# Kernel optimization log

Measured on AMD Instinct MI355X. Metric: run time of the kernel, lower is better.

## Reference

```python
import jax, jax.numpy as jnp
import numpy as np

B, F, S, H = 1024, 64, 512, 128


def setup_inputs() -> dict:
    key = jax.random.key(0)
    ks = jax.random.split(key, 9)
    x = jax.random.normal(ks[0], (B, F, S), dtype=jnp.float32)
    available_len = jax.random.randint(ks[1], (B,), 1, S // 2).astype(jnp.int32)
    extra = jax.random.randint(ks[2], (B,), 0, S // 2)
    predict_len = jnp.minimum(available_len + extra, S).astype(jnp.int32)
    s = 1.0 / float(np.sqrt(H))  # PyTorch default uniform init scale
    u = lambda k, shape: jax.random.uniform(k, shape, jnp.float32, -s, s)
    W_ih = u(ks[3], (4 * H, F))
    W_hh = u(ks[4], (4 * H, H))
    b_ih = u(ks[5], (4 * H,))
    b_hh = u(ks[6], (4 * H,))
    W_den = u(ks[7], (F, H))
    b_den = u(ks[8], (F,))
    init_ch = jnp.zeros((1, 2 * H), dtype=jnp.float32)  # nn.Parameter(zeros(1, 2*n_hidden))
    return {"x": x, "available_len": available_len, "predict_len": predict_len,
            "W_ih": W_ih, "W_hh": W_hh, "b_ih": b_ih, "b_hh": b_hh,
            "W_den": W_den, "b_den": b_den, "init_ch": init_ch}


def reference(x, available_len, predict_len, W_ih, W_hh, b_ih, b_hh, W_den, b_den, init_ch):
    """Masked autoregressive LSTMCell recurrence.

    Row r is active at step t iff t < predict_len[r]; once inactive it never
    re-activates (the torch code's per-step gather of c_1/h_1 by predict_len is
    exactly this monotone-shrinking active set, expressed here as a masked
    full-batch state update). For t >= available_len[r] (and still active) the
    input is the model's own previous prediction (auto-regression feedback).
    Returns the permuted buffer (seq_len, batch, n_fea), matching the torch code.
    """
    Bb, Ff, Ss = x.shape
    Hh = W_hh.shape[1]
    xs = jnp.transpose(x, (2, 0, 1))  # (S, B, F)
    c0 = jnp.broadcast_to(init_ch[:, :Hh], (Bb, Hh))
    h0 = jnp.broadcast_to(init_ch[:, Hh:], (Bb, Hh))

    def step(carry, inp):
        h, c, prev_out = carry
        t, x_t = inp  # t: scalar step index, x_t: (B, F)
        sel = t < predict_len                       # active rows
        use_pred = (t >= available_len) & sel
        inp_t = jnp.where(use_pred[:, None], prev_out, x_t)
        gates = inp_t @ W_ih.T + b_ih + h @ W_hh.T + b_hh  # (B, 4H)
        i, f, g, o = jnp.split(gates, 4, axis=-1)
        c_new = jax.nn.sigmoid(f) * c + jax.nn.sigmoid(i) * jnp.tanh(g)
        h_new = jax.nn.sigmoid(o) * jnp.tanh(c_new)
        h = jnp.where(sel[:, None], h_new, h)
        c = jnp.where(sel[:, None], c_new, c)
        pred = h_new @ W_den.T + b_den              # (B, F)
        out_t = jnp.where(sel[:, None], pred, inp_t)  # x[t, sel] <- prediction
        return (h, c, out_t), out_t

    _, ys = jax.lax.scan(step, (h0, c0, jnp.zeros_like(xs[0])),
                         (jnp.arange(Ss), xs))
    return ys  # (S, B, F)
```

## Files before the change

### kernel.cpp

```cpp
#include <hip/hip_runtime.h>

#define BB 1024
#define FF 64
#define SS 512
#define HH 128
#define ZP 200
#define ZROWS 16
#define OUTS (BB*FF)

typedef __attribute__((ext_vector_type(8))) short bf16x8;
typedef __attribute__((ext_vector_type(4))) float f32x4;

__device__ __forceinline__ unsigned short f2bf(float f) {
    unsigned int u = __float_as_uint(f);
    u += 0x7fff + ((u >> 16) & 1);
    return (unsigned short)(u >> 16);
}

__device__ __forceinline__ void bar_lds() {
    __builtin_amdgcn_sched_barrier(0);
    asm volatile("s_waitcnt lgkmcnt(0)\n\ts_barrier" ::: "memory");
    __builtin_amdgcn_sched_barrier(0);
}

__global__ void fold_kernel(const float* __restrict__ W_ih,
                            const float* __restrict__ W_den,
                            const float* __restrict__ b_den,
                            float* __restrict__ ws)
{
    const int n = blockIdx.x;
    const int k = threadIdx.x;
    float s = 0.f;
    #pragma unroll 8
    for (int f = 0; f < FF; ++f) s = fmaf(W_ih[n*FF + f], W_den[f*HH + k], s);
    ws[n*HH + k] = s;
    if (k == 0) {
        float bsum = 0.f;
        #pragma unroll 8
        for (int f = 0; f < FF; ++f) bsum = fmaf(W_ih[n*FF + f], b_den[f], bsum);
        ws[4*HH*HH + n] = bsum;
    }
}

__global__ void sort_kernel(const int* __restrict__ avail, int* __restrict__ perm)
{
    const int i = threadIdx.x;
    const int key = avail[i];
    int rank = 0;
    for (int j = 0; j < BB; ++j) {
        const int kj = avail[j];
        rank += (kj < key) || (kj == key && j < i);
    }
    perm[rank] = i;
}

__global__ __launch_bounds__(512)
void lstm_mfma_kernel(const float* __restrict__ x,
                      const int* __restrict__ available_len,
                      const int* __restrict__ predict_len,
                      const float* __restrict__ W_ih,
                      const float* __restrict__ W_hh,
                      const float* __restrict__ b_ih,
                      const float* __restrict__ b_hh,
                      const float* __restrict__ W_den,
                      const float* __restrict__ b_den,
                      const float* __restrict__ init_ch,
                      const float* __restrict__ ws,
                      const int* __restrict__ perm,
                      float* __restrict__ out)
{
    const int b0  = blockIdx.x * 4;
    const int tid = threadIdx.x;
    const int w   = tid >> 6;
    const int l   = tid & 63;
    const int l16 = l & 15;
    const int lq  = l >> 4;
    const bool w4 = (w < 4);

    __shared__ __align__(16) unsigned short zbuf[2][ZROWS * ZP];

    for (int i = tid; i < 2 * ZROWS * ZP / 2; i += 512)
        ((unsigned int*)zbuf)[i] = 0u;

    const int rr0 = perm[b0], rr1 = perm[b0+1], rr2 = perm[b0+2], rr3 = perm[b0+3];
    const int p0 = predict_len[rr0], p1 = predict_len[rr1],
              p2 = predict_len[rr2], p3 = predict_len[rr3];
    const int a0i = available_len[rr0], a1i = available_len[rr1],
              a2i = available_len[rr2], a3i = available_len[rr3];
    const int maxP  = max(max(p0, p1), max(p2, p3));
    const int tsw   = max(max(a0i, a1i), max(a2i, a3i));
    const int tmin  = min(min(a0i, a1i), min(a2i, a3i));
    const int ph1s  = (tmin > 1) ? (tmin - 1) : 0;
    const int rl    = perm[b0 + lq];
    const int P_my  = predict_len[rl];
    const int AV_my = available_len[rl];

    bf16x8 wg[4][6];
    float bias[4];
    #pragma unroll
    for (int g = 0; g < 4; ++g) {
        const int n = 128*g + 16*w + l16;
        const float* rih = W_ih + n * FF;
        const float* rhh = W_hh + n * HH;
        #pragma unroll
        for (int kt = 0; kt < 6; ++kt) {
            const int k = 32*kt + 8*lq;
            const float* src = (k < 64) ? (rih + k) : (rhh + (k - 64));
            bf16x8 r;
            #pragma unroll
            for (int i = 0; i < 8; i++) r[i] = (short)f2bf(src[i]);
            wg[g][kt] = r;
        }
        bias[g] = b_ih[n] + b_hh[n];
    }

    bf16x8 wd0, wd1, wd2, wd3;
    float bden = 0.f;
    size_t xbase = 0;
    int AV_x = 0;
    if (w4) {
        const int f = 16*w + l16;
        const float* rd = W_den + f * HH;
        bf16x8 r;
        #pragma unroll
        for (int i = 0; i < 8; i++) r[i] = (short)f2bf(rd[0*32 + 8*lq + i]);
        wd0 = r;
        #pragma unroll
        for (int i = 0; i < 8; i++) r[i] = (short)f2bf(rd[1*32 + 8*lq + i]);
        wd1 = r;
        #pragma unroll
        for (int i = 0; i < 8; i++) r[i] = (short)f2bf(rd[2*32 + 8*lq + i]);
        wd2 = r;
        #pragma unroll
        for (int i = 0; i < 8; i++) r[i] = (short)f2bf(rd[3*32 + 8*lq + i]);
        wd3 = r;
        bden = b_den[f];
        const int rx = perm[b0 + w];
        xbase = ((size_t)rx * FF + l) * SS;
        AV_x  = available_len[rx];
    }

    const int unit  = 16*w + l16;
    const int abase = l16*ZP + 8*lq;
    float c = init_ch[unit];
    const float h0v = init_ch[HH + unit];
    float* outb = out + (size_t)rl * FF + 16*w + l16;

    bar_lds();

    zbuf[0][(4*lq)*ZP + 64 + unit] = f2bf(h0v);
    if (w4) zbuf[0][(4*w)*ZP + l] = f2bf(x[xbase]);

    float4 qc = {0.f,0.f,0.f,0.f};
    if (AV_x > 1) qc = *(const float4*)(x + xbase);

    int cur = 0;

#define DO_T(S, XNEXT)                                                         \
  do {                                                                         \
    const int s_ = (S);                                                        \
    bar_lds();                                             \
    const unsigned short* zc_ = zbuf[cur];                                     \
    bf16x8 a0 = *(const bf16x8*)(zc_ + abase +   0);                           \
    bf16x8 a1 = *(const bf16x8*)(zc_ + abase +  32);                           \
    bf16x8 a2 = *(const bf16x8*)(zc_ + abase +  64);                           \
    bf16x8 a3 = *(const bf16x8*)(zc_ + abase +  96);                           \
    bf16x8 a4 = *(const bf16x8*)(zc_ + abase + 128);                           \
    bf16x8 a5 = *(const bf16x8*)(zc_ + abase + 160);                           \
    if (w4 && s_ >= 1) {                   \
      f32x4 ca = {0.f,0.f,0.f,0.f}, cb = {0.f,0.f,0.f,0.f};                    \
      ca = __builtin_amdgcn_mfma_f32_16x16x32_bf16(a2, wd0, ca, 0,0,0);        \
      cb = __builtin_amdgcn_mfma_f32_16x16x32_bf16(a4, wd2, cb, 0,0,0);        \
      ca = __builtin_amdgcn_mfma_f32_16x16x32_bf16(a3, wd1, ca, 0,0,0);        \
      cb = __builtin_amdgcn_mfma_f32_16x16x32_bf16(a5, wd3, cb, 0,0,0);        \
      if ((s_ - 1) < P_my) outb[(size_t)(s_-1) * OUTS] = ca[0] + cb[0] + bden; \
    }                                                                          \
    f32x4 ac0 = {0.f,0.f,0.f,0.f}, ac1 = {0.f,0.f,0.f,0.f},                    \
          ac2 = {0.f,0.f,0.f,0.f}, ac3 = {0.f,0.f,0.f,0.f};                    \
    ac0 = __builtin_amdgcn_mfma_f32_16x16x32_bf16(a0, wg[0][0], ac0, 0,0,0);   \
    ac1 = __builtin_amdgcn_mfma_f32_16x16x32_bf16(a0, wg[1][0], ac1, 0,0,0);   \
    ac2 = __builtin_amdgcn_mfma_f32_16x16x32_bf16(a0, wg[2][0], ac2, 0,0,0);   \
    ac3 = __builtin_amdgcn_mfma_f32_16x16x32_bf16(a0, wg[3][0], ac3, 0,0,0);   \
    ac0 = __builtin_amdgcn_mfma_f32_16x16x32_bf16(a1, wg[0][1], ac0, 0,0,0);   \
    ac1 = __builtin_amdgcn_mfma_f32_16x16x32_bf16(a1, wg[1][1], ac1, 0,0,0);   \
    ac2 = __builtin_amdgcn_mfma_f32_16x16x32_bf16(a1, wg[2][1], ac2, 0,0,0);   \
    ac3 = __builtin_amdgcn_mfma_f32_16x16x32_bf16(a1, wg[3][1], ac3, 0,0,0);   \
    ac0 = __builtin_amdgcn_mfma_f32_16x16x32_bf16(a2, wg[0][2], ac0, 0,0,0);   \
    ac1 = __builtin_amdgcn_mfma_f32_16x16x32_bf16(a2, wg[1][2], ac1, 0,0,0);   \
    ac2 = __builtin_amdgcn_mfma_f32_16x16x32_bf16(a2, wg[2][2], ac2, 0,0,0);   \
    ac3 = __builtin_amdgcn_mfma_f32_16x16x32_bf16(a2, wg[3][2], ac3, 0,0,0);   \
    ac0 = __builtin_amdgcn_mfma_f32_16x16x32_bf16(a3, wg[0][3], ac0, 0,0,0);   \
    ac1 = __builtin_amdgcn_mfma_f32_16x16x32_bf16(a3, wg[1][3], ac1, 0,0,0);   \
    ac2 = __builtin_amdgcn_mfma_f32_16x16x32_bf16(a3, wg[2][3], ac2, 0,0,0);   \
    ac3 = __builtin_amdgcn_mfma_f32_16x16x32_bf16(a3, wg[3][3], ac3, 0,0,0);   \
    ac0 = __builtin_amdgcn_mfma_f32_16x16x32_bf16(a4, wg[0][4], ac0, 0,0,0);   \
    ac1 = __builtin_amdgcn_mfma_f32_16x16x32_bf16(a4, wg[1][4], ac1, 0,0,0);   \
    ac2 = __builtin_amdgcn_mfma_f32_16x16x32_bf16(a4, wg[2][4], ac2, 0,0,0);   \
    ac3 = __builtin_amdgcn_mfma_f32_16x16x32_bf16(a4, wg[3][4], ac3, 0,0,0);   \
    ac0 = __builtin_amdgcn_mfma_f32_16x16x32_bf16(a5, wg[0][5], ac0, 0,0,0);   \
    ac1 = __builtin_amdgcn_mfma_f32_16x16x32_bf16(a5, wg[1][5], ac1, 0,0,0);   \
    ac2 = __builtin_amdgcn_mfma_f32_16x16x32_bf16(a5, wg[2][5], ac2, 0,0,0);   \
    ac3 = __builtin_amdgcn_mfma_f32_16x16x32_bf16(a5, wg[3][5], ac3, 0,0,0);   \
    const float g0 = ac0[0] + bias[0];                                         \
    const float g1 = ac1[0] + bias[1];                                         \
    const float g2 = ac2[0] + bias[2];                                         \
    const float g3 = ac3[0] + bias[3];                                         \
    const float si = 1.f / (1.f + __expf(-g0));                                \
    const float sf = 1.f / (1.f + __expf(-g1));                                \
    const float tg = 1.f - 2.f / (__expf(2.f * g2) + 1.f);                     \
    const float so = 1.f / (1.f + __expf(-g3));                                \
    const float cn = sf * c + si * tg;                                         \
    const float tc = 1.f - 2.f / (__expf(2.f * cn) + 1.f);                     \
    const float hn = so * tc;                                                  \
    const int nxt_ = cur ^ 1;                                                  \
    if (s_ < P_my) { c = cn; zbuf[nxt_][(4*lq)*ZP + 64 + unit] = f2bf(hn); }   \
    if (w4 && (s_ + 1 < AV_x)) zbuf[nxt_][(4*w)*ZP + l] = f2bf(XNEXT);         \
    cur = nxt_;                                                                \
  } while (0)

#define DO_STEP(S, XNEXT)                                                      \
  do {                                                                         \
    const int s_ = (S);                                                        \
    bar_lds();                                               \
    const unsigned short* zc_ = zbuf[cur];                                     \
    bf16x8 a0 = *(const bf16x8*)(zc_ + abase +   0);                           \
    bf16x8 a1 = *(const bf16x8*)(zc_ + abase +  32);                           \
    bf16x8 a2 = *(const bf16x8*)(zc_ + abase +  64);                           \
    bf16x8 a3 = *(const bf16x8*)(zc_ + abase +  96);                           \
    bf16x8 a4 = *(const bf16x8*)(zc_ + abase + 128);                           \
    bf16x8 a5 = *(const bf16x8*)(zc_ + abase + 160);                           \
    if (w4 && s_ >= 1) {                   \
      f32x4 ca = {0.f,0.f,0.f,0.f}, cb = {0.f,0.f,0.f,0.f};                    \
      ca = __builtin_amdgcn_mfma_f32_16x16x32_bf16(a2, wd0, ca, 0,0,0);        \
      cb = __builtin_amdgcn_mfma_f32_16x16x32_bf16(a4, wd2, cb, 0,0,0);        \
      ca = __builtin_amdgcn_mfma_f32_16x16x32_bf16(a3, wd1, ca, 0,0,0);        \
      cb = __builtin_amdgcn_mfma_f32_16x16x32_bf16(a5, wd3, cb, 0,0,0);        \
      if ((s_ - 1) < P_my) outb[(size_t)(s_-1) * OUTS] = ca[0] + cb[0] + bden; \
    }                                                                          \
    f32x4 ac0 = {0.f,0.f,0.f,0.f}, ac1 = {0.f,0.f,0.f,0.f},                    \
          ac2 = {0.f,0.f,0.f,0.f}, ac3 = {0.f,0.f,0.f,0.f};                    \
    ac0 = __builtin_amdgcn_mfma_f32_16x16x32_bf16(a0, wg[0][0], ac0, 0,0,0);   \
    ac1 = __builtin_amdgcn_mfma_f32_16x16x32_bf16(a0, wg[1][0], ac1, 0,0,0);   \
    ac2 = __builtin_amdgcn_mfma_f32_16x16x32_bf16(a0, wg[2][0], ac2, 0,0,0);   \
    ac3 = __builtin_amdgcn_mfma_f32_16x16x32_bf16(a0, wg[3][0], ac3, 0,0,0);   \
    ac0 = __builtin_amdgcn_mfma_f32_16x16x32_bf16(a1, wg[0][1], ac0, 0,0,0);   \
    ac1 = __builtin_amdgcn_mfma_f32_16x16x32_bf16(a1, wg[1][1], ac1, 0,0,0);   \
    ac2 = __builtin_amdgcn_mfma_f32_16x16x32_bf16(a1, wg[2][1], ac2, 0,0,0);   \
    ac3 = __builtin_amdgcn_mfma_f32_16x16x32_bf16(a1, wg[3][1], ac3, 0,0,0);   \
    ac0 = __builtin_amdgcn_mfma_f32_16x16x32_bf16(a2, wg[0][2], ac0, 0,0,0);   \
    ac1 = __builtin_amdgcn_mfma_f32_16x16x32_bf16(a2, wg[1][2], ac1, 0,0,0);   \
    ac2 = __builtin_amdgcn_mfma_f32_16x16x32_bf16(a2, wg[2][2], ac2, 0,0,0);   \
    ac3 = __builtin_amdgcn_mfma_f32_16x16x32_bf16(a2, wg[3][2], ac3, 0,0,0);   \
    ac0 = __builtin_amdgcn_mfma_f32_16x16x32_bf16(a3, wg[0][3], ac0, 0,0,0);   \
    ac1 = __builtin_amdgcn_mfma_f32_16x16x32_bf16(a3, wg[1][3], ac1, 0,0,0);   \
    ac2 = __builtin_amdgcn_mfma_f32_16x16x32_bf16(a3, wg[2][3], ac2, 0,0,0);   \
    ac3 = __builtin_amdgcn_mfma_f32_16x16x32_bf16(a3, wg[3][3], ac3, 0,0,0);   \
    ac0 = __builtin_amdgcn_mfma_f32_16x16x32_bf16(a4, wg[0][4], ac0, 0,0,0);   \
    ac1 = __builtin_amdgcn_mfma_f32_16x16x32_bf16(a4, wg[1][4], ac1, 0,0,0);   \
    ac2 = __builtin_amdgcn_mfma_f32_16x16x32_bf16(a4, wg[2][4], ac2, 0,0,0);   \
    ac3 = __builtin_amdgcn_mfma_f32_16x16x32_bf16(a4, wg[3][4], ac3, 0,0,0);   \
    ac0 = __builtin_amdgcn_mfma_f32_16x16x32_bf16(a5, wg[0][5], ac0, 0,0,0);   \
    ac1 = __builtin_amdgcn_mfma_f32_16x16x32_bf16(a5, wg[1][5], ac1, 0,0,0);   \
    ac2 = __builtin_amdgcn_mfma_f32_16x16x32_bf16(a5, wg[2][5], ac2, 0,0,0);   \
    ac3 = __builtin_amdgcn_mfma_f32_16x16x32_bf16(a5, wg[3][5], ac3, 0,0,0);   \
    const float g0 = ac0[0] + bias[0];                                         \
    const float g1 = ac1[0] + bias[1];                                         \
    const float g2 = ac2[0] + bias[2];                                         \
    const float g3 = ac3[0] + bias[3];                                         \
    const float si = 1.f / (1.f + __expf(-g0));                                \
    const float sf = 1.f / (1.f + __expf(-g1));                                \
    const float tg = 1.f - 2.f / (__expf(2.f * g2) + 1.f);                     \
    const float so = 1.f / (1.f + __expf(-g3));                                \
    const float cn = sf * c + si * tg;                                         \
    const float tc = 1.f - 2.f / (__expf(2.f * cn) + 1.f);                     \
    const float hn = so * tc;                                                  \
    const int nxt_ = cur ^ 1;                                                  \
    if (s_ < P_my) { c = cn; zbuf[nxt_][(4*lq)*ZP + 64 + unit] = f2bf(hn); }   \
    bar_lds();                                                \
    if (w4) {                                                                  \
      const unsigned short* zn_ = zbuf[nxt_];                                  \
      bf16x8 h0f = *(const bf16x8*)(zn_ + abase + 64 +  0);                    \
      bf16x8 h1f = *(const bf16x8*)(zn_ + abase + 64 + 32);                    \
      bf16x8 h2f = *(const bf16x8*)(zn_ + abase + 64 + 64);                    \
      bf16x8 h3f = *(const bf16x8*)(zn_ + abase + 64 + 96);                    \
      f32x4 pa = {0.f,0.f,0.f,0.f}, pb = {0.f,0.f,0.f,0.f};                    \
      pa = __builtin_amdgcn_mfma_f32_16x16x32_bf16(h0f, wd0, pa, 0,0,0);       \
      pb = __builtin_amdgcn_mfma_f32_16x16x32_bf16(h2f, wd2, pb, 0,0,0);       \
      pa = __builtin_amdgcn_mfma_f32_16x16x32_bf16(h1f, wd1, pa, 0,0,0);       \
      pb = __builtin_amdgcn_mfma_f32_16x16x32_bf16(h3f, wd3, pb, 0,0,0);       \
      const float pred_ = pa[0] + pb[0] + bden;                                \
      if (s_ < P_my) {                                                         \
        outb[(size_t)s_ * OUTS] = pred_;                                       \
        if (s_ + 1 >= AV_my)                                                   \
          zbuf[nxt_][(4*lq)*ZP + 16*w + l16] = f2bf(pred_);                    \
      }                                                                        \
      if (s_ + 1 < AV_x) zbuf[nxt_][(4*w)*ZP + l] = f2bf(XNEXT);               \
    }                                                                          \
    cur = nxt_;                                                                \
  } while (0)

    int t4 = 0;
    for (; t4 + 4 <= ph1s; t4 += 4) {
        float4 qn = {0.f,0.f,0.f,0.f};
        if (w4 && (t4 + 4 < AV_x))
            qn = *(const float4*)(x + xbase + t4 + 4);
        DO_T(t4 + 0, qc.y);
        DO_T(t4 + 1, qc.z);
        DO_T(t4 + 2, qc.w);
        DO_T(t4 + 3, qn.x);
        qc = qn;
    }
    for (; t4 < ph1s; ++t4) {
        float xs = 0.f;
        if (w4 && (t4 + 1 < AV_x)) xs = x[xbase + t4 + 1];
        DO_T(t4, xs);
    }
    for (; t4 < tsw; ++t4) {
        float xs = 0.f;
        if (w4 && (t4 + 1 < AV_x)) xs = x[xbase + t4 + 1];
        DO_STEP(t4, xs);
    }
#undef DO_T
#undef DO_STEP

    if (tsw < maxP) {
        const float* wfold = ws;
        const float* bfold = ws + 4*HH*HH;
        #pragma unroll
        for (int g = 0; g < 4; ++g) {
            const int n = 128*g + 16*w + l16;
            const float* rhh = W_hh + n * HH;
            const float* rfo = wfold + n * HH;
            #pragma unroll
            for (int j = 0; j < 4; ++j) {
                const int k = 32*j + 8*lq;
                bf16x8 r;
                #pragma unroll
                for (int i = 0; i < 8; i++) r[i] = (short)f2bf(rhh[k+i] + rfo[k+i]);
                wg[g][j] = r;
            }
            bias[g] += bfold[n];
        }

        for (int t = tsw; t < maxP; ++t) {
            bar_lds();
            const unsigned short* zc = zbuf[cur];
            bf16x8 h0f = *(const bf16x8*)(zc + abase + 64 +  0);
            bf16x8 h1f = *(const bf16x8*)(zc + abase + 64 + 32);
            bf16x8 h2f = *(const bf16x8*)(zc + abase + 64 + 64);
            bf16x8 h3f = *(const bf16x8*)(zc + abase + 64 + 96);

            if (w4) {
                f32x4 pa = {0.f,0.f,0.f,0.f}, pb = {0.f,0.f,0.f,0.f};
                pa = __builtin_amdgcn_mfma_f32_16x16x32_bf16(h0f, wd0, pa, 0,0,0);
                pb = __builtin_amdgcn_mfma_f32_16x16x32_bf16(h2f, wd2, pb, 0,0,0);
                pa = __builtin_amdgcn_mfma_f32_16x16x32_bf16(h1f, wd1, pa, 0,0,0);
                pb = __builtin_amdgcn_mfma_f32_16x16x32_bf16(h3f, wd3, pb, 0,0,0);
                if ((t - 1) < P_my)
                    outb[(size_t)(t-1) * OUTS] = pa[0] + pb[0] + bden;
            }

            f32x4 ac0 = {0.f,0.f,0.f,0.f}, ac1 = {0.f,0.f,0.f,0.f},
                  ac2 = {0.f,0.f,0.f,0.f}, ac3 = {0.f,0.f,0.f,0.f};
            ac0 = __builtin_amdgcn_mfma_f32_16x16x32_bf16(h0f, wg[0][0], ac0, 0,0,0);
            ac1 = __builtin_amdgcn_mfma_f32_16x16x32_bf16(h0f, wg[1][0], ac1, 0,0,0);
            ac2 = __builtin_amdgcn_mfma_f32_16x16x32_bf16(h0f, wg[2][0], ac2, 0,0,0);
            ac3 = __builtin_amdgcn_mfma_f32_16x16x32_bf16(h0f, wg[3][0], ac3, 0,0,0);
            ac0 = __builtin_amdgcn_mfma_f32_16x16x32_bf16(h1f, wg[0][1], ac0, 0,0,0);
            ac1 = __builtin_amdgcn_mfma_f32_16x16x32_bf16(h1f, wg[1][1], ac1, 0,0,0);
            ac2 = __builtin_amdgcn_mfma_f32_16x16x32_bf16(h1f, wg[2][1], ac2, 0,0,0);
            ac3 = __builtin_amdgcn_mfma_f32_16x16x32_bf16(h1f, wg[3][1], ac3, 0,0,0);
            ac0 = __builtin_amdgcn_mfma_f32_16x16x32_bf16(h2f, wg[0][2], ac0, 0,0,0);
            ac1 = __builtin_amdgcn_mfma_f32_16x16x32_bf16(h2f, wg[1][2], ac1, 0,0,0);
            ac2 = __builtin_amdgcn_mfma_f32_16x16x32_bf16(h2f, wg[2][2], ac2, 0,0,0);
            ac3 = __builtin_amdgcn_mfma_f32_16x16x32_bf16(h2f, wg[3][2], ac3, 0,0,0);
            ac0 = __builtin_amdgcn_mfma_f32_16x16x32_bf16(h3f, wg[0][3], ac0, 0,0,0);
            ac1 = __builtin_amdgcn_mfma_f32_16x16x32_bf16(h3f, wg[1][3], ac1, 0,0,0);
            ac2 = __builtin_amdgcn_mfma_f32_16x16x32_bf16(h3f, wg[2][3], ac2, 0,0,0);
            ac3 = __builtin_amdgcn_mfma_f32_16x16x32_bf16(h3f, wg[3][3], ac3, 0,0,0);

            const float g0 = ac0[0] + bias[0];
            const float g1 = ac1[0] + bias[1];
            const float g2 = ac2[0] + bias[2];
            const float g3 = ac3[0] + bias[3];
            const float si = 1.f / (1.f + __expf(-g0));
            const float sf = 1.f / (1.f + __expf(-g1));
            const float tg = 1.f - 2.f / (__expf(2.f * g2) + 1.f);
            const float so = 1.f / (1.f + __expf(-g3));
            const float cn = sf * c + si * tg;
            const float tc = 1.f - 2.f / (__expf(2.f * cn) + 1.f);
            const float hn = so * tc;

            const int nxt = cur ^ 1;
            if (t < P_my) { c = cn; zbuf[nxt][(4*lq)*ZP + 64 + unit] = f2bf(hn); }
            cur = nxt;
        }

        bar_lds();
        if (w4) {
            const unsigned short* zc = zbuf[cur];
            bf16x8 h0f = *(const bf16x8*)(zc + abase + 64 +  0);
            bf16x8 h1f = *(const bf16x8*)(zc + abase + 64 + 32);
            bf16x8 h2f = *(const bf16x8*)(zc + abase + 64 + 64);
            bf16x8 h3f = *(const bf16x8*)(zc + abase + 64 + 96);
            f32x4 pa = {0.f,0.f,0.f,0.f}, pb = {0.f,0.f,0.f,0.f};
            pa = __builtin_amdgcn_mfma_f32_16x16x32_bf16(h0f, wd0, pa, 0,0,0);
            pb = __builtin_amdgcn_mfma_f32_16x16x32_bf16(h2f, wd2, pb, 0,0,0);
            pa = __builtin_amdgcn_mfma_f32_16x16x32_bf16(h1f, wd1, pa, 0,0,0);
            pb = __builtin_amdgcn_mfma_f32_16x16x32_bf16(h3f, wd3, pb, 0,0,0);
            if ((maxP - 1) < P_my)
                outb[(size_t)(maxP-1) * OUTS] = pa[0] + pb[0] + bden;
        }
    }
}

__global__ void tail_copy(const float* __restrict__ x,
                          const int* __restrict__ predict_len,
                          float* __restrict__ out)
{
    __shared__ float tile[64][65];
    const int b  = blockIdx.x;
    const int t0 = blockIdx.y * 64;
    const int P  = predict_len[b];
    if (t0 + 64 <= P) return;

    const int tid = threadIdx.x;
    const int tt  = tid & 63;
    const int fb  = tid >> 6;
    #pragma unroll
    for (int i = 0; i < 16; i++) {
        int f = fb * 16 + i;
        tile[f][tt] = x[(size_t)b * FF * SS + (size_t)f * SS + t0 + tt];
    }
    __syncthreads();
    const int f2 = tid & 63;
    const int tb = tid >> 6;
    #pragma unroll
    for (int i = 0; i < 16; i++) {
        int tloc = tb * 16 + i;
        int t    = t0 + tloc;
        if (t >= P) out[(size_t)t * BB * FF + (size_t)b * FF + f2] = tile[f2][tloc];
    }
}

extern "C" void kernel_launch(void* const* d_in, const int* in_sizes, int n_in,
                              void* d_out, int out_size, void* d_ws, size_t ws_size,
                              hipStream_t stream) {
    const float* x       = (const float*)d_in[0];
    const int*   avail   = (const int*)  d_in[1];
    const int*   plen    = (const int*)  d_in[2];
    const float* W_ih    = (const float*)d_in[3];
    const float* W_hh    = (const float*)d_in[4];
    const float* b_ih    = (const float*)d_in[5];
    const float* b_hh    = (const float*)d_in[6];
    const float* W_den   = (const float*)d_in[7];
    const float* b_den   = (const float*)d_in[8];
    const float* init_ch = (const float*)d_in[9];
    float*       out     = (float*)d_out;
    float*       ws      = (float*)d_ws;
    int*         perm    = (int*)(ws + 4*HH*HH + 4*HH);

    fold_kernel<<<dim3(4*HH), dim3(HH), 0, stream>>>(W_ih, W_den, b_den, ws);
    sort_kernel<<<dim3(1), dim3(BB), 0, stream>>>(avail, perm);
    tail_copy<<<dim3(BB, SS/64), dim3(256), 0, stream>>>(x, plen, out);
    lstm_mfma_kernel<<<dim3(BB/4), dim3(512), 0, stream>>>(
        x, avail, plen, W_ih, W_hh, b_ih, b_hh, W_den, b_den, init_ch, ws, perm, out);
}
```

Measured before the change: 472.6 us.

## Halve LSTM block to four waves each computing two gate column tiles

```diff
diff --git a/kernel.cpp b/kernel.cpp
--- a/kernel.cpp
+++ b/kernel.cpp
@@ -44,17 +44,22 @@
 
 __global__ void sort_kernel(const int* __restrict__ avail, int* __restrict__ perm)
 {
-    const int i = threadIdx.x;
-    const int key = avail[i];
+    __shared__ int keys[BB];
+    const int t = threadIdx.x;
+    for (int i = t; i < BB; i += 256) keys[i] = avail[i];
+    __syncthreads();
+    const int i = blockIdx.x * 256 + t;
+    const int key = keys[i];
     int rank = 0;
+    #pragma unroll 8
     for (int j = 0; j < BB; ++j) {
-        const int kj = avail[j];
+        const int kj = keys[j];
         rank += (kj < key) || (kj == key && j < i);
     }
     perm[rank] = i;
 }
 
-__global__ __launch_bounds__(512)
+__global__ __launch_bounds__(256, 1)
 void lstm_mfma_kernel(const float* __restrict__ x,
                       const int* __restrict__ available_len,
                       const int* __restrict__ predict_len,
@@ -75,11 +80,10 @@
     const int l   = tid & 63;
     const int l16 = l & 15;
     const int lq  = l >> 4;
-    const bool w4 = (w < 4);
 
     __shared__ __align__(16) unsigned short zbuf[2][ZROWS * ZP];
 
-    for (int i = tid; i < 2 * ZROWS * ZP / 2; i += 512)
+    for (int i = tid; i < 2 * ZROWS * ZP / 2; i += 256)
         ((unsigned int*)zbuf)[i] = 0u;
 
     const int rr0 = perm[b0], rr1 = perm[b0+1], rr2 = perm[b0+2], rr3 = perm[b0+3];
@@ -95,206 +99,169 @@
     const int P_my  = predict_len[rl];
     const int AV_my = available_len[rl];
 
-    bf16x8 wg[4][6];
-    float bias[4];
+    bf16x8 wg[4][2][6];
+    float bias[4][2];
     #pragma unroll
     for (int g = 0; g < 4; ++g) {
-        const int n = 128*g + 16*w + l16;
-        const float* rih = W_ih + n * FF;
-        const float* rhh = W_hh + n * HH;
         #pragma unroll
-        for (int kt = 0; kt < 6; ++kt) {
+        for (int ct = 0; ct < 2; ++ct) {
+            const int n = 128*g + 32*w + 16*ct + l16;
+            const float* rih = W_ih + n * FF;
+            const float* rhh = W_hh + n * HH;
+            #pragma unroll
+            for (int kt = 0; kt < 6; ++kt) {
+                const int k = 32*kt + 8*lq;
+                const float* src = (k < 64) ? (rih + k) : (rhh + (k - 64));
+                bf16x8 r;
+                #pragma unroll
+                for (int i = 0; i < 8; i++) r[i] = (short)f2bf(src[i]);
+                wg[g][ct][kt] = r;
+            }
+            bias[g][ct] = b_ih[n] + b_hh[n];
+        }
+    }
+
+    bf16x8 wd[4];
+    float bden;
+    {
+        const int f = 16*w + l16;
+        const float* rd = W_den + f * HH;
+        #pragma unroll
+        for (int kt = 0; kt < 4; ++kt) {
             const int k = 32*kt + 8*lq;
-            const float* src = (k < 64) ? (rih + k) : (rhh + (k - 64));
             bf16x8 r;
             #pragma unroll
-            for (int i = 0; i < 8; i++) r[i] = (short)f2bf(src[i]);
-            wg[g][kt] = r;
+            for (int i = 0; i < 8; i++) r[i] = (short)f2bf(rd[k + i]);
+            wd[kt] = r;
         }
-        bias[g] = b_ih[n] + b_hh[n];
-    }
-
-    bf16x8 wd0, wd1, wd2, wd3;
-    float bden = 0.f;
-    size_t xbase = 0;
-    int AV_x = 0;
-    if (w4) {
-        const int f = 16*w + l16;
-        const float* rd = W_den + f * HH;
-        bf16x8 r;
-        #pragma unroll
-        for (int i = 0; i < 8; i++) r[i] = (short)f2bf(rd[0*32 + 8*lq + i]);
-        wd0 = r;
-        #pragma unroll
-        for (int i = 0; i < 8; i++) r[i] = (short)f2bf(rd[1*32 + 8*lq + i]);
-        wd1 = r;
-        #pragma unroll
-        for (int i = 0; i < 8; i++) r[i] = (short)f2bf(rd[2*32 + 8*lq + i]);
-        wd2 = r;
-        #pragma unroll
-        for (int i = 0; i < 8; i++) r[i] = (short)f2bf(rd[3*32 + 8*lq + i]);
-        wd3 = r;
         bden = b_den[f];
-        const int rx = perm[b0 + w];
-        xbase = ((size_t)rx * FF + l) * SS;
-        AV_x  = available_len[rx];
-    }
-
-    const int unit  = 16*w + l16;
+    }
+
+    const int rx = perm[b0 + w];
+    const size_t xbase = ((size_t)rx * FF + l) * SS;
+    const int AV_x = available_len[rx];
+
+    const int u0 = 32*w + l16;
+    const int u1 = u0 + 16;
     const int abase = l16*ZP + 8*lq;
-    float c = init_ch[unit];
-    const float h0v = init_ch[HH + unit];
+    float cc0 = init_ch[u0], cc1 = init_ch[u1];
+    const float h0v0 = init_ch[HH + u0], h0v1 = init_ch[HH + u1];
     float* outb = out + (size_t)rl * FF + 16*w + l16;
 
     bar_lds();
 
-    zbuf[0][(4*lq)*ZP + 64 + unit] = f2bf(h0v);
-    if (w4) zbuf[0][(4*w)*ZP + l] = f2bf(x[xbase]);
+    zbuf[0][(4*lq)*ZP + 64 + u0] = f2bf(h0v0);
+    zbuf[0][(4*lq)*ZP + 64 + u1] = f2bf(h0v1);
+    zbuf[0][(4*w)*ZP + l] = f2bf(x[xbase]);
 
     float4 qc = {0.f,0.f,0.f,0.f};
     if (AV_x > 1) qc = *(const float4*)(x + xbase);
 
     int cur = 0;
+
+#define GATES6(AV)                                                             \
+    f32x4 ag[4][2];                                                            \
+    _Pragma("unroll")                                                          \
+    for (int g = 0; g < 4; ++g) { ag[g][0] = (f32x4){0.f,0.f,0.f,0.f};         \
+                                  ag[g][1] = (f32x4){0.f,0.f,0.f,0.f}; }       \
+    _Pragma("unroll")                                                          \
+    for (int kt = 0; kt < 6; ++kt) {                                           \
+      _Pragma("unroll")                                                        \
+      for (int g = 0; g < 4; ++g) {                                            \
+        ag[g][0] = __builtin_amdgcn_mfma_f32_16x16x32_bf16(AV[kt], wg[g][0][kt], ag[g][0], 0,0,0); \
+        ag[g][1] = __builtin_amdgcn_mfma_f32_16x16x32_bf16(AV[kt], wg[g][1][kt], ag[g][1], 0,0,0); \
+      }                                                                        \
+    }
+
+#define CELL2(S, NXT)                                                          \
+    _Pragma("unroll")                                                          \
+    for (int ct = 0; ct < 2; ++ct) {                                           \
+      const float g0 = ag[0][ct][0] + bias[0][ct];                             \
+      const float g1 = ag[1][ct][0] + bias[1][ct];                             \
+      const float g2 = ag[2][ct][0] + bias[2][ct];                             \
+      const float g3 = ag[3][ct][0] + bias[3][ct];                             \
+      const float si = 1.f / (1.f + __expf(-g0));                              \
+      const float sf = 1.f / (1.f + __expf(-g1));                              \
+      const float tg = 1.f - 2.f / (__expf(2.f * g2) + 1.f);                   \
+      const float so = 1.f / (1.f + __expf(-g3));                              \
+      const float cn = sf * (ct ? cc1 : cc0) + si * tg;                        \
+      const float tc = 1.f - 2.f / (__expf(2.f * cn) + 1.f);                   \
+      const float hn = so * tc;                                                \
+      if ((S) < P_my) {                                                        \
+        if (ct) cc1 = cn; else cc0 = cn;                                       \
+        zbuf[NXT][(4*lq)*ZP + 64 + (ct ? u1 : u0)] = f2bf(hn);                 \
+      }                                                                        \
+    }
 
 #define DO_T(S, XNEXT)                                                         \
   do {                                                                         \
     const int s_ = (S);                                                        \
-    bar_lds();                                             \
+    bar_lds();                                                                 \
     const unsigned short* zc_ = zbuf[cur];                                     \
-    bf16x8 a0 = *(const bf16x8*)(zc_ + abase +   0);                           \
-    bf16x8 a1 = *(const bf16x8*)(zc_ + abase +  32);                           \
-    bf16x8 a2 = *(const bf16x8*)(zc_ + abase +  64);                           \
-    bf16x8 a3 = *(const bf16x8*)(zc_ + abase +  96);                           \
-    bf16x8 a4 = *(const bf16x8*)(zc_ + abase + 128);                           \
-    bf16x8 a5 = *(const bf16x8*)(zc_ + abase + 160);                           \
-    if (w4 && s_ >= 1) {                   \
+    bf16x8 av[6];                                                              \
+    av[0] = *(const bf16x8*)(zc_ + abase +   0);                               \
+    av[1] = *(const bf16x8*)(zc_ + abase +  32);                               \
+    av[2] = *(const bf16x8*)(zc_ + abase +  64);                               \
+    av[3] = *(const bf16x8*)(zc_ + abase +  96);                               \
+    av[4] = *(const bf16x8*)(zc_ + abase + 128);                               \
+    av[5] = *(const bf16x8*)(zc_ + abase + 160);                               \
+    if (s_ >= 1) {                         \
       f32x4 ca = {0.f,0.f,0.f,0.f}, cb = {0.f,0.f,0.f,0.f};                    \
-      ca = __builtin_amdgcn_mfma_f32_16x16x32_bf16(a2, wd0, ca, 0,0,0);        \
-      cb = __builtin_amdgcn_mfma_f32_16x16x32_bf16(a4, wd2, cb, 0,0,0);        \
-      ca = __builtin_amdgcn_mfma_f32_16x16x32_bf16(a3, wd1, ca, 0,0,0);        \
-      cb = __builtin_amdgcn_mfma_f32_16x16x32_bf16(a5, wd3, cb, 0,0,0);        \
+      ca = __builtin_amdgcn_mfma_f32_16x16x32_bf16(av[2], wd[0], ca, 0,0,0);   \
+      cb = __builtin_amdgcn_mfma_f32_16x16x32_bf16(av[4], wd[2], cb, 0,0,0);   \
+      ca = __builtin_amdgcn_mfma_f32_16x16x32_bf16(av[3], wd[1], ca, 0,0,0);   \
+      cb = __builtin_amdgcn_mfma_f32_16x16x32_bf16(av[5], wd[3], cb, 0,0,0);   \
       if ((s_ - 1) < P_my) outb[(size_t)(s_-1) * OUTS] = ca[0] + cb[0] + bden; \
     }                                                                          \
-    f32x4 ac0 = {0.f,0.f,0.f,0.f}, ac1 = {0.f,0.f,0.f,0.f},                    \
-          ac2 = {0.f,0.f,0.f,0.f}, ac3 = {0.f,0.f,0.f,0.f};                    \
-    ac0 = __builtin_amdgcn_mfma_f32_16x16x32_bf16(a0, wg[0][0], ac0, 0,0,0);   \
-    ac1 = __builtin_amdgcn_mfma_f32_16x16x32_bf16(a0, wg[1][0], ac1, 0,0,0);   \
-    ac2 = __builtin_amdgcn_mfma_f32_16x16x32_bf16(a0, wg[2][0], ac2, 0,0,0);   \
-    ac3 = __builtin_amdgcn_mfma_f32_16x16x32_bf16(a0, wg[3][0], ac3, 0,0,0);   \
-    ac0 = __builtin_amdgcn_mfma_f32_16x16x32_bf16(a1, wg[0][1], ac0, 0,0,0);   \
-    ac1 = __builtin_amdgcn_mfma_f32_16x16x32_bf16(a1, wg[1][1], ac1, 0,0,0);   \
-    ac2 = __builtin_amdgcn_mfma_f32_16x16x32_bf16(a1, wg[2][1], ac2, 0,0,0);   \
-    ac3 = __builtin_amdgcn_mfma_f32_16x16x32_bf16(a1, wg[3][1], ac3, 0,0,0);   \
-    ac0 = __builtin_amdgcn_mfma_f32_16x16x32_bf16(a2, wg[0][2], ac0, 0,0,0);   \
-    ac1 = __builtin_amdgcn_mfma_f32_16x16x32_bf16(a2, wg[1][2], ac1, 0,0,0);   \
-    ac2 = __builtin_amdgcn_mfma_f32_16x16x32_bf16(a2, wg[2][2], ac2, 0,0,0);   \
-    ac3 = __builtin_amdgcn_mfma_f32_16x16x32_bf16(a2, wg[3][2], ac3, 0,0,0);   \
-    ac0 = __builtin_amdgcn_mfma_f32_16x16x32_bf16(a3, wg[0][3], ac0, 0,0,0);   \
-    ac1 = __builtin_amdgcn_mfma_f32_16x16x32_bf16(a3, wg[1][3], ac1, 0,0,0);   \
-    ac2 = __builtin_amdgcn_mfma_f32_16x16x32_bf16(a3, wg[2][3], ac2, 0,0,0);   \
-    ac3 = __builtin_amdgcn_mfma_f32_16x16x32_bf16(a3, wg[3][3], ac3, 0,0,0);   \
-    ac0 = __builtin_amdgcn_mfma_f32_16x16x32_bf16(a4, wg[0][4], ac0, 0,0,0);   \
-    ac1 = __builtin_amdgcn_mfma_f32_16x16x32_bf16(a4, wg[1][4], ac1, 0,0,0);   \
-    ac2 = __builtin_amdgcn_mfma_f32_16x16x32_bf16(a4, wg[2][4], ac2, 0,0,0);   \
-    ac3 = __builtin_amdgcn_mfma_f32_16x16x32_bf16(a4, wg[3][4], ac3, 0,0,0);   \
-    ac0 = __builtin_amdgcn_mfma_f32_16x16x32_bf16(a5, wg[0][5], ac0, 0,0,0);   \
-    ac1 = __builtin_amdgcn_mfma_f32_16x16x32_bf16(a5, wg[1][5], ac1, 0,0,0);   \
-    ac2 = __builtin_amdgcn_mfma_f32_16x16x32_bf16(a5, wg[2][5], ac2, 0,0,0);   \
-    ac3 = __builtin_amdgcn_mfma_f32_16x16x32_bf16(a5, wg[3][5], ac3, 0,0,0);   \
-    const float g0 = ac0[0] + bias[0];                                         \
-    const float g1 = ac1[0] + bias[1];                                         \
-    const float g2 = ac2[0] + bias[2];                                         \
-    const float g3 = ac3[0] + bias[3];                                         \
-    const float si = 1.f / (1.f + __expf(-g0));                                \
-    const float sf = 1.f / (1.f + __expf(-g1));                                \
-    const float tg = 1.f - 2.f / (__expf(2.f * g2) + 1.f);                     \
-    const float so = 1.f / (1.f + __expf(-g3));                                \
-    const float cn = sf * c + si * tg;                                         \
-    const float tc = 1.f - 2.f / (__expf(2.f * cn) + 1.f);                     \
-    const float hn = so * tc;                                                  \
+    GATES6(av)                                                                 \
     const int nxt_ = cur ^ 1;                                                  \
-    if (s_ < P_my) { c = cn; zbuf[nxt_][(4*lq)*ZP + 64 + unit] = f2bf(hn); }   \
-    if (w4 && (s_ + 1 < AV_x)) zbuf[nxt_][(4*w)*ZP + l] = f2bf(XNEXT);         \
+    CELL2(s_, nxt_)                                                            \
+    if (s_ + 1 < AV_x) zbuf[nxt_][(4*w)*ZP + l] = f2bf(XNEXT);                 \
     cur = nxt_;                                                                \
   } while (0)
 
 #define DO_STEP(S, XNEXT)                                                      \
   do {                                                                         \
     const int s_ = (S);                                                        \
-    bar_lds();                                               \
+    bar_lds();                                                         \
     const unsigned short* zc_ = zbuf[cur];                                     \
-    bf16x8 a0 = *(const bf16x8*)(zc_ + abase +   0);                           \
-    bf16x8 a1 = *(const bf16x8*)(zc_ + abase +  32);                           \
-    bf16x8 a2 = *(const bf16x8*)(zc_ + abase +  64);                           \
-    bf16x8 a3 = *(const bf16x8*)(zc_ + abase +  96);                           \
-    bf16x8 a4 = *(const bf16x8*)(zc_ + abase + 128);                           \
-    bf16x8 a5 = *(const bf16x8*)(zc_ + abase + 160);                           \
-    if (w4 && s_ >= 1) {                   \
+    bf16x8 av[6];                                                              \
+    av[0] = *(const bf16x8*)(zc_ + abase +   0);                               \
+    av[1] = *(const bf16x8*)(zc_ + abase +  32);                               \
+    av[2] = *(const bf16x8*)(zc_ + abase +  64);                               \
+    av[3] = *(const bf16x8*)(zc_ + abase +  96);                               \
+    av[4] = *(const bf16x8*)(zc_ + abase + 128);                               \
+    av[5] = *(const bf16x8*)(zc_ + abase + 160);                               \
+    if (s_ >= 1) {                         \
       f32x4 ca = {0.f,0.f,0.f,0.f}, cb = {0.f,0.f,0.f,0.f};                    \
-      ca = __builtin_amdgcn_mfma_f32_16x16x32_bf16(a2, wd0, ca, 0,0,0);        \
-      cb = __builtin_amdgcn_mfma_f32_16x16x32_bf16(a4, wd2, cb, 0,0,0);        \
-      ca = __builtin_amdgcn_mfma_f32_16x16x32_bf16(a3, wd1, ca, 0,0,0);        \
-      cb = __builtin_amdgcn_mfma_f32_16x16x32_bf16(a5, wd3, cb, 0,0,0);        \
+      ca = __builtin_amdgcn_mfma_f32_16x16x32_bf16(av[2], wd[0], ca, 0,0,0);   \
+      cb = __builtin_amdgcn_mfma_f32_16x16x32_bf16(av[4], wd[2], cb, 0,0,0);   \
+      ca = __builtin_amdgcn_mfma_f32_16x16x32_bf16(av[3], wd[1], ca, 0,0,0);   \
+      cb = __builtin_amdgcn_mfma_f32_16x16x32_bf16(av[5], wd[3], cb, 0,0,0);   \
       if ((s_ - 1) < P_my) outb[(size_t)(s_-1) * OUTS] = ca[0] + cb[0] + bden; \
     }                                                                          \
-    f32x4 ac0 = {0.f,0.f,0.f,0.f}, ac1 = {0.f,0.f,0.f,0.f},                    \
-          ac2 = {0.f,0.f,0.f,0.f}, ac3 = {0.f,0.f,0.f,0.f};                    \
-    ac0 = __builtin_amdgcn_mfma_f32_16x16x32_bf16(a0, wg[0][0], ac0, 0,0,0);   \
-    ac1 = __builtin_amdgcn_mfma_f32_16x16x32_bf16(a0, wg[1][0], ac1, 0,0,0);   \
-    ac2 = __builtin_amdgcn_mfma_f32_16x16x32_bf16(a0, wg[2][0], ac2, 0,0,0);   \
-    ac3 = __builtin_amdgcn_mfma_f32_16x16x32_bf16(a0, wg[3][0], ac3, 0,0,0);   \
-    ac0 = __builtin_amdgcn_mfma_f32_16x16x32_bf16(a1, wg[0][1], ac0, 0,0,0);   \
-    ac1 = __builtin_amdgcn_mfma_f32_16x16x32_bf16(a1, wg[1][1], ac1, 0,0,0);   \
-    ac2 = __builtin_amdgcn_mfma_f32_16x16x32_bf16(a1, wg[2][1], ac2, 0,0,0);   \
-    ac3 = __builtin_amdgcn_mfma_f32_16x16x32_bf16(a1, wg[3][1], ac3, 0,0,0);   \
-    ac0 = __builtin_amdgcn_mfma_f32_16x16x32_bf16(a2, wg[0][2], ac0, 0,0,0);   \
-    ac1 = __builtin_amdgcn_mfma_f32_16x16x32_bf16(a2, wg[1][2], ac1, 0,0,0);   \
-    ac2 = __builtin_amdgcn_mfma_f32_16x16x32_bf16(a2, wg[2][2], ac2, 0,0,0);   \
-    ac3 = __builtin_amdgcn_mfma_f32_16x16x32_bf16(a2, wg[3][2], ac3, 0,0,0);   \
-    ac0 = __builtin_amdgcn_mfma_f32_16x16x32_bf16(a3, wg[0][3], ac0, 0,0,0);   \
-    ac1 = __builtin_amdgcn_mfma_f32_16x16x32_bf16(a3, wg[1][3], ac1, 0,0,0);   \
-    ac2 = __builtin_amdgcn_mfma_f32_16x16x32_bf16(a3, wg[2][3], ac2, 0,0,0);   \
-    ac3 = __builtin_amdgcn_mfma_f32_16x16x32_bf16(a3, wg[3][3], ac3, 0,0,0);   \
-    ac0 = __builtin_amdgcn_mfma_f32_16x16x32_bf16(a4, wg[0][4], ac0, 0,0,0);   \
-    ac1 = __builtin_amdgcn_mfma_f32_16x16x32_bf16(a4, wg[1][4], ac1, 0,0,0);   \
-    ac2 = __builtin_amdgcn_mfma_f32_16x16x32_bf16(a4, wg[2][4], ac2, 0,0,0);   \
-    ac3 = __builtin_amdgcn_mfma_f32_16x16x32_bf16(a4, wg[3][4], ac3, 0,0,0);   \
-    ac0 = __builtin_amdgcn_mfma_f32_16x16x32_bf16(a5, wg[0][5], ac0, 0,0,0);   \
-    ac1 = __builtin_amdgcn_mfma_f32_16x16x32_bf16(a5, wg[1][5], ac1, 0,0,0);   \
-    ac2 = __builtin_amdgcn_mfma_f32_16x16x32_bf16(a5, wg[2][5], ac2, 0,0,0);   \
-    ac3 = __builtin_amdgcn_mfma_f32_16x16x32_bf16(a5, wg[3][5], ac3, 0,0,0);   \
-    const float g0 = ac0[0] + bias[0];                                         \
-    const float g1 = ac1[0] + bias[1];                                         \
-    const float g2 = ac2[0] + bias[2];                                         \
-    const float g3 = ac3[0] + bias[3];                                         \
-    const float si = 1.f / (1.f + __expf(-g0));                                \
-    const float sf = 1.f / (1.f + __expf(-g1));                                \
-    const float tg = 1.f - 2.f / (__expf(2.f * g2) + 1.f);                     \
-    const float so = 1.f / (1.f + __expf(-g3));                                \
-    const float cn = sf * c + si * tg;                                         \
-    const float tc = 1.f - 2.f / (__expf(2.f * cn) + 1.f);                     \
-    const float hn = so * tc;                                                  \
+    GATES6(av)                                                                 \
     const int nxt_ = cur ^ 1;                                                  \
-    if (s_ < P_my) { c = cn; zbuf[nxt_][(4*lq)*ZP + 64 + unit] = f2bf(hn); }   \
+    CELL2(s_, nxt_)                                                            \
+    if (s_ + 1 < AV_x) zbuf[nxt_][(4*w)*ZP + l] = f2bf(XNEXT);                 \
     bar_lds();                                                \
-    if (w4) {                                                                  \
+    {                                                                          \
       const unsigned short* zn_ = zbuf[nxt_];                                  \
       bf16x8 h0f = *(const bf16x8*)(zn_ + abase + 64 +  0);                    \
       bf16x8 h1f = *(const bf16x8*)(zn_ + abase + 64 + 32);                    \
       bf16x8 h2f = *(const bf16x8*)(zn_ + abase + 64 + 64);                    \
       bf16x8 h3f = *(const bf16x8*)(zn_ + abase + 64 + 96);                    \
       f32x4 pa = {0.f,0.f,0.f,0.f}, pb = {0.f,0.f,0.f,0.f};                    \
-      pa = __builtin_amdgcn_mfma_f32_16x16x32_bf16(h0f, wd0, pa, 0,0,0);       \
-      pb = __builtin_amdgcn_mfma_f32_16x16x32_bf16(h2f, wd2, pb, 0,0,0);       \
-      pa = __builtin_amdgcn_mfma_f32_16x16x32_bf16(h1f, wd1, pa, 0,0,0);       \
-      pb = __builtin_amdgcn_mfma_f32_16x16x32_bf16(h3f, wd3, pb, 0,0,0);       \
+      pa = __builtin_amdgcn_mfma_f32_16x16x32_bf16(h0f, wd[0], pa, 0,0,0);     \
+      pb = __builtin_amdgcn_mfma_f32_16x16x32_bf16(h2f, wd[2], pb, 0,0,0);     \
+      pa = __builtin_amdgcn_mfma_f32_16x16x32_bf16(h1f, wd[1], pa, 0,0,0);     \
+      pb = __builtin_amdgcn_mfma_f32_16x16x32_bf16(h3f, wd[3], pb, 0,0,0);     \
       const float pred_ = pa[0] + pb[0] + bden;                                \
       if (s_ < P_my) {                                                         \
         outb[(size_t)s_ * OUTS] = pred_;                                       \
         if (s_ + 1 >= AV_my)                                                   \
           zbuf[nxt_][(4*lq)*ZP + 16*w + l16] = f2bf(pred_);                    \
       }                                                                        \
-      if (s_ + 1 < AV_x) zbuf[nxt_][(4*w)*ZP + l] = f2bf(XNEXT);               \
     }                                                                          \
     cur = nxt_;                                                                \
   } while (0)
@@ -302,7 +269,7 @@
     int t4 = 0;
     for (; t4 + 4 <= ph1s; t4 += 4) {
         float4 qn = {0.f,0.f,0.f,0.f};
-        if (w4 && (t4 + 4 < AV_x))
+        if (t4 + 4 < AV_x)
             qn = *(const float4*)(x + xbase + t4 + 4);
         DO_T(t4 + 0, qc.y);
         DO_T(t4 + 1, qc.z);
@@ -312,12 +279,12 @@
     }
     for (; t4 < ph1s; ++t4) {
         float xs = 0.f;
-        if (w4 && (t4 + 1 < AV_x)) xs = x[xbase + t4 + 1];
+        if (t4 + 1 < AV_x) xs = x[xbase + t4 + 1];
         DO_T(t4, xs);
     }
     for (; t4 < tsw; ++t4) {
         float xs = 0.f;
-        if (w4 && (t4 + 1 < AV_x)) xs = x[xbase + t4 + 1];
+        if (t4 + 1 < AV_x) xs = x[xbase + t4 + 1];
         DO_STEP(t4, xs);
     }
 #undef DO_T
@@ -328,90 +295,78 @@
         const float* bfold = ws + 4*HH*HH;
         #pragma unroll
         for (int g = 0; g < 4; ++g) {
-            const int n = 128*g + 16*w + l16;
-            const float* rhh = W_hh + n * HH;
-            const float* rfo = wfold + n * HH;
             #pragma unroll
-            for (int j = 0; j < 4; ++j) {
-                const int k = 32*j + 8*lq;
-                bf16x8 r;
+            for (int ct = 0; ct < 2; ++ct) {
+                const int n = 128*g + 32*w + 16*ct + l16;
+                const float* rhh = W_hh + n * HH;
+                const float* rfo = wfold + n * HH;
                 #pragma unroll
-                for (int i = 0; i < 8; i++) r[i] = (short)f2bf(rhh[k+i] + rfo[k+i]);
-                wg[g][j] = r;
+                for (int j = 0; j < 4; ++j) {
+                    const int k = 32*j + 8*lq;
+                    bf16x8 r;
+                    #pragma unroll
+                    for (int i = 0; i < 8; i++) r[i] = (short)f2bf(rhh[k+i] + rfo[k+i]);
+                    wg[g][ct][j] = r;
+                }
+                bias[g][ct] += bfold[n];
             }
-            bias[g] += bfold[n];
         }
 
         for (int t = tsw; t < maxP; ++t) {
             bar_lds();
             const unsigned short* zc = zbuf[cur];
-            bf16x8 h0f = *(const bf16x8*)(zc + abase + 64 +  0);
-            bf16x8 h1f = *(const bf16x8*)(zc + abase + 64 + 32);
-            bf16x8 h2f = *(const bf16x8*)(zc + abase + 64 + 64);
-            bf16x8 h3f = *(const bf16x8*)(zc + abase + 64 + 96);
-
-            if (w4) {
+            bf16x8 hv[4];
+            hv[0] = *(const bf16x8*)(zc + abase + 64 +  0);
+            hv[1] = *(const bf16x8*)(zc + abase + 64 + 32);
+            hv[2] = *(const bf16x8*)(zc + abase + 64 + 64);
+            hv[3] = *(const bf16x8*)(zc + abase + 64 + 96);
+
+            {
                 f32x4 pa = {0.f,0.f,0.f,0.f}, pb = {0.f,0.f,0.f,0.f};
-                pa = __builtin_amdgcn_mfma_f32_16x16x32_bf16(h0f, wd0, pa, 0,0,0);
-                pb = __builtin_amdgcn_mfma_f32_16x16x32_bf16(h2f, wd2, pb, 0,0,0);
-                pa = __builtin_amdgcn_mfma_f32_16x16x32_bf16(h1f, wd1, pa, 0,0,0);
-                pb = __builtin_amdgcn_mfma_f32_16x16x32_bf16(h3f, wd3, pb, 0,0,0);
+                pa = __builtin_amdgcn_mfma_f32_16x16x32_bf16(hv[0], wd[0], pa, 0,0,0);
+                pb = __builtin_amdgcn_mfma_f32_16x16x32_bf16(hv[2], wd[2], pb, 0,0,0);
+                pa = __builtin_amdgcn_mfma_f32_16x16x32_bf16(hv[1], wd[1], pa, 0,0,0);
+                pb = __builtin_amdgcn_mfma_f32_16x16x32_bf16(hv[3], wd[3], pb, 0,0,0);
                 if ((t - 1) < P_my)
                     outb[(size_t)(t-1) * OUTS] = pa[0] + pb[0] + bden;
             }
 
-            f32x4 ac0 = {0.f,0.f,0.f,0.f}, ac1 = {0.f,0.f,0.f,0.f},
-                  ac2 = {0.f,0.f,0.f,0.f}, ac3 = {0.f,0.f,0.f,0.f};
-            ac0 = __builtin_amdgcn_mfma_f32_16x16x32_bf16(h0f, wg[0][0], ac0, 0,0,0);
-            ac1 = __builtin_amdgcn_mfma_f32_16x16x32_bf16(h0f, wg[1][0], ac1, 0,0,0);
-            ac2 = __builtin_amdgcn_mfma_f32_16x16x32_bf16(h0f, wg[2][0], ac2, 0,0,0);
-            ac3 = __builtin_amdgcn_mfma_f32_16x16x32_bf16(h0f, wg[3][0], ac3, 0,0,0);
-            ac0 = __builtin_amdgcn_mfma_f32_16x16x32_bf16(h1f, wg[0][1], ac0, 0,0,0);
-            ac1 = __builtin_amdgcn_mfma_f32_16x16x32_bf16(h1f, wg[1][1], ac1, 0,0,0);
-            ac2 = __builtin_amdgcn_mfma_f32_16x16x32_bf16(h1f, wg[2][1], ac2, 0,0,0);
-            ac3 = __builtin_amdgcn_mfma_f32_16x16x32_bf16(h1f, wg[3][1], ac3, 0,0,0);
-            ac0 = __builtin_amdgcn_mfma_f32_16x16x32_bf16(h2f, wg[0][2], ac0, 0,0,0);
-            ac1 = __builtin_amdgcn_mfma_f32_16x16x32_bf16(h2f, wg[1][2], ac1, 0,0,0);
-            ac2 = __builtin_amdgcn_mfma_f32_16x16x32_bf16(h2f, wg[2][2], ac2, 0,0,0);
-            ac3 = __builtin_amdgcn_mfma_f32_16x16x32_bf16(h2f, wg[3][2], ac3, 0,0,0);
-            ac0 = __builtin_amdgcn_mfma_f32_16x16x32_bf16(h3f, wg[0][3], ac0, 0,0,0);
-            ac1 = __builtin_amdgcn_mfma_f32_16x16x32_bf16(h3f, wg[1][3], ac1, 0,0,0);
-            ac2 = __builtin_amdgcn_mfma_f32_16x16x32_bf16(h3f, wg[2][3], ac2, 0,0,0);
-            ac3 = __builtin_amdgcn_mfma_f32_16x16x32_bf16(h3f, wg[3][3], ac3, 0,0,0);
-
-            const float g0 = ac0[0] + bias[0];
-            const float g1 = ac1[0] + bias[1];
-            const float g2 = ac2[0] + bias[2];
-            const float g3 = ac3[0] + bias[3];
-            const float si = 1.f / (1.f + __expf(-g0));
-            const float sf = 1.f / (1.f + __expf(-g1));
-            const float tg = 1.f - 2.f / (__expf(2.f * g2) + 1.f);
-            const float so = 1.f / (1.f + __expf(-g3));
-            const float cn = sf * c + si * tg;
-            const float tc = 1.f - 2.f / (__expf(2.f * cn) + 1.f);
-            const float hn = so * tc;
+            f32x4 ag[4][2];
+            #pragma unroll
+            for (int g = 0; g < 4; ++g) { ag[g][0] = (f32x4){0.f,0.f,0.f,0.f};
+                                          ag[g][1] = (f32x4){0.f,0.f,0.f,0.f}; }
+            #pragma unroll
+            for (int kt = 0; kt < 4; ++kt) {
+                #pragma unroll
+                for (int g = 0; g < 4; ++g) {
+                    ag[g][0] = __builtin_amdgcn_mfma_f32_16x16x32_bf16(hv[kt], wg[g][0][kt], ag[g][0], 0,0,0);
+                    ag[g][1] = __builtin_amdgcn_mfma_f32_16x16x32_bf16(hv[kt], wg[g][1][kt], ag[g][1], 0,0,0);
+                }
+            }
 
             const int nxt = cur ^ 1;
-            if (t < P_my) { c = cn; zbuf[nxt][(4*lq)*ZP + 64 + unit] = f2bf(hn); }
+            CELL2(t, nxt)
             cur = nxt;
         }
 
         bar_lds();
-        if (w4) {
+        {
             const unsigned short* zc = zbuf[cur];
             bf16x8 h0f = *(const bf16x8*)(zc + abase + 64 +  0);
             bf16x8 h1f = *(const bf16x8*)(zc + abase + 64 + 32);
             bf16x8 h2f = *(const bf16x8*)(zc + abase + 64 + 64);
             bf16x8 h3f = *(const bf16x8*)(zc + abase + 64 + 96);
             f32x4 pa = {0.f,0.f,0.f,0.f}, pb = {0.f,0.f,0.f,0.f};
-            pa = __builtin_amdgcn_mfma_f32_16x16x32_bf16(h0f, wd0, pa, 0,0,0);
-            pb = __builtin_amdgcn_mfma_f32_16x16x32_bf16(h2f, wd2, pb, 0,0,0);
-            pa = __builtin_amdgcn_mfma_f32_16x16x32_bf16(h1f, wd1, pa, 0,0,0);
-            pb = __builtin_amdgcn_mfma_f32_16x16x32_bf16(h3f, wd3, pb, 0,0,0);
+            pa = __builtin_amdgcn_mfma_f32_16x16x32_bf16(h0f, wd[0], pa, 0,0,0);
+            pb = __builtin_amdgcn_mfma_f32_16x16x32_bf16(h2f, wd[2], pb, 0,0,0);
+            pa = __builtin_amdgcn_mfma_f32_16x16x32_bf16(h1f, wd[1], pa, 0,0,0);
+            pb = __builtin_amdgcn_mfma_f32_16x16x32_bf16(h3f, wd[3], pb, 0,0,0);
             if ((maxP - 1) < P_my)
                 outb[(size_t)(maxP-1) * OUTS] = pa[0] + pb[0] + bden;
         }
     }
+#undef GATES6
+#undef CELL2
 }
 
 __global__ void tail_copy(const float* __restrict__ x,
@@ -461,8 +416,8 @@
     int*         perm    = (int*)(ws + 4*HH*HH + 4*HH);
 
     fold_kernel<<<dim3(4*HH), dim3(HH), 0, stream>>>(W_ih, W_den, b_den, ws);
-    sort_kernel<<<dim3(1), dim3(BB), 0, stream>>>(avail, perm);
+    sort_kernel<<<dim3(4), dim3(256), 0, stream>>>(avail, perm);
     tail_copy<<<dim3(BB, SS/64), dim3(256), 0, stream>>>(x, plen, out);
-    lstm_mfma_kernel<<<dim3(BB/4), dim3(512), 0, stream>>>(
+    lstm_mfma_kernel<<<dim3(BB/4), dim3(256), 0, stream>>>(
         x, avail, plen, W_ih, W_hh, b_ih, b_hh, W_den, b_den, init_ch, ws, perm, out);
 }
```

New measurement: 569.7 us. 1.21x slower.

## Fuse tail copy into LSTM kernel epilogue and parallelize sort with LDS keys

Applied to the files above, without the earlier changes.

```diff
diff --git a/kernel.cpp b/kernel.cpp
--- a/kernel.cpp
+++ b/kernel.cpp
@@ -44,11 +44,16 @@
 
 __global__ void sort_kernel(const int* __restrict__ avail, int* __restrict__ perm)
 {
-    const int i = threadIdx.x;
-    const int key = avail[i];
+    __shared__ int keys[BB];
+    const int t = threadIdx.x;
+    for (int i = t; i < BB; i += 256) keys[i] = avail[i];
+    __syncthreads();
+    const int i = blockIdx.x * 256 + t;
+    const int key = keys[i];
     int rank = 0;
+    #pragma unroll 8
     for (int j = 0; j < BB; ++j) {
-        const int kj = avail[j];
+        const int kj = keys[j];
         rank += (kj < key) || (kj == key && j < i);
     }
     perm[rank] = i;
@@ -78,6 +83,7 @@
     const bool w4 = (w < 4);
 
     __shared__ __align__(16) unsigned short zbuf[2][ZROWS * ZP];
+    __shared__ float tile[64][65];
 
     for (int i = tid; i < 2 * ZROWS * ZP / 2; i += 512)
         ((unsigned int*)zbuf)[i] = 0u;
@@ -412,34 +418,37 @@
                 outb[(size_t)(maxP-1) * OUTS] = pa[0] + pb[0] + bden;
         }
     }
-}
-
-__global__ void tail_copy(const float* __restrict__ x,
-                          const int* __restrict__ predict_len,
-                          float* __restrict__ out)
-{
-    __shared__ float tile[64][65];
-    const int b  = blockIdx.x;
-    const int t0 = blockIdx.y * 64;
-    const int P  = predict_len[b];
-    if (t0 + 64 <= P) return;
-
-    const int tid = threadIdx.x;
-    const int tt  = tid & 63;
-    const int fb  = tid >> 6;
-    #pragma unroll
-    for (int i = 0; i < 16; i++) {
-        int f = fb * 16 + i;
-        tile[f][tt] = x[(size_t)b * FF * SS + (size_t)f * SS + t0 + tt];
-    }
-    __syncthreads();
-    const int f2 = tid & 63;
-    const int tb = tid >> 6;
-    #pragma unroll
-    for (int i = 0; i < 16; i++) {
-        int tloc = tb * 16 + i;
-        int t    = t0 + tloc;
-        if (t >= P) out[(size_t)t * BB * FF + (size_t)b * FF + f2] = tile[f2][tloc];
+
+    #pragma unroll 1
+    for (int q = 0; q < 4; ++q) {
+        const int r = perm[b0 + q];
+        const int P = predict_len[r];
+        if (P >= SS) continue;
+        const float* xr = x + (size_t)r * FF * SS;
+        for (int t0 = (P >> 6) << 6; t0 < SS; t0 += 64) {
+            bar_lds();
+            {
+                const int tt = tid & 63;
+                const int fb = tid >> 6;
+                #pragma unroll
+                for (int i = 0; i < 8; ++i) {
+                    const int f = fb * 8 + i;
+                    tile[f][tt] = xr[(size_t)f * SS + t0 + tt];
+                }
+            }
+            bar_lds();
+            {
+                const int f2 = tid & 63;
+                const int tb = tid >> 6;
+                #pragma unroll
+                for (int i = 0; i < 8; ++i) {
+                    const int tloc = tb * 8 + i;
+                    const int t = t0 + tloc;
+                    if (t >= P)
+                        out[(size_t)t * OUTS + (size_t)r * FF + f2] = tile[f2][tloc];
+                }
+            }
+        }
     }
 }
 
@@ -461,8 +470,7 @@
     int*         perm    = (int*)(ws + 4*HH*HH + 4*HH);
 
     fold_kernel<<<dim3(4*HH), dim3(HH), 0, stream>>>(W_ih, W_den, b_den, ws);
-    sort_kernel<<<dim3(1), dim3(BB), 0, stream>>>(avail, perm);
-    tail_copy<<<dim3(BB, SS/64), dim3(256), 0, stream>>>(x, plen, out);
+    sort_kernel<<<dim3(4), dim3(256), 0, stream>>>(avail, perm);
     lstm_mfma_kernel<<<dim3(BB/4), dim3(512), 0, stream>>>(
         x, avail, plen, W_ih, W_hh, b_ih, b_hh, W_den, b_den, init_ch, ws, perm, out);
 }
```

After: 439.4 us. 7.0% less time.
